# Kernel optimization log

Measured on AMD Instinct MI355X. Metric: run time of the kernel, lower is better.

## Reference

```python
import jax, jax.numpy as jnp
import numpy as np

DIST_MULT = 0.1
CLIP_LOW = 0.0
EPS = 1e-6


def setup_inputs() -> dict:
    key = jax.random.key(0)
    k1, _ = jax.random.split(key)
    x_msg_binned = jax.random.normal(k1, (8, 64, 512, 16), dtype=jnp.float32)
    msk = jnp.ones((8, 64, 512, 1), dtype=jnp.float32)
    return {"x_msg_binned": x_msg_binned, "msk": msk}


def reference(x_msg_binned, msk):
    # A: (B, bins, N, F) masked node features
    A = x_msg_binned * msk
    na = jnp.sum(A * A, axis=-1)  # (B, bins, N)
    # Gram matrix: (B, bins, N, N)
    G = jnp.einsum("bknf,bkmf->bknm", A, A)
    D = jnp.sqrt(jnp.maximum(na[..., :, None] - 2.0 * G + na[..., None, :], EPS))
    dm = jnp.exp(-DIST_MULT * D)[..., None]  # (B, bins, N, N, 1)
    return jnp.clip(dm, CLIP_LOW, 1.0)
```

## Files before the change

kernel.cpp:

```cpp
#include <hip/hip_runtime.h>


typedef float f32x4 __attribute__((ext_vector_type(4)));

#define NEG_DIST_LOG2E (-0.14426950408889634f)
#define EPS_F 1e-6f

__global__ __launch_bounds__(256) void node_pair_gaussian_kernel(
    const float* __restrict__ x,
    const float* __restrict__ msk,
    float* __restrict__ out)
{
    __shared__ __align__(16) float lds_n[16][128];
    __shared__ __align__(16) float lds_m[16][128];
    __shared__ __align__(16) float na_n[128];
    __shared__ __align__(16) float na_m[128];

    const int tid   = threadIdx.x;
    const int tile  = blockIdx.x;
    const int slice = blockIdx.y;
    const int n0 = (tile >> 2) << 7;
    const int m0 = (tile & 3) << 7;

    const float* xs = x   + (size_t)slice * (512 * 16);
    const float* ms = msk + (size_t)slice * 512;

    #pragma unroll
    for (int it = 0; it < 2; ++it) {
        const int task = tid + it * 256;
        const int node = task & 127;
        const int f4   = task >> 7;
        {
            const f32x4 v = *(const f32x4*)(xs + (size_t)(n0 + node) * 16 + f4 * 4);
            const float mm = ms[n0 + node];
            lds_n[f4 * 4 + 0][node] = v.x * mm;
            lds_n[f4 * 4 + 1][node] = v.y * mm;
            lds_n[f4 * 4 + 2][node] = v.z * mm;
            lds_n[f4 * 4 + 3][node] = v.w * mm;
        }
        {
            const f32x4 v = *(const f32x4*)(xs + (size_t)(m0 + node) * 16 + f4 * 4);
            const float mm = ms[m0 + node];
            lds_m[f4 * 4 + 0][node] = v.x * mm;
            lds_m[f4 * 4 + 1][node] = v.y * mm;
            lds_m[f4 * 4 + 2][node] = v.z * mm;
            lds_m[f4 * 4 + 3][node] = v.w * mm;
        }
    }
    __syncthreads();

    {
        const int node = tid & 127;
        float s = 0.0f;
        if (tid < 128) {
            #pragma unroll
            for (int f = 0; f < 16; ++f) s = fmaf(lds_m[f][node], lds_m[f][node], s);
            na_m[node] = s;
        } else {
            #pragma unroll
            for (int f = 0; f < 16; ++f) s = fmaf(lds_n[f][node], lds_n[f][node], s);
            na_n[node] = s;
        }
    }
    __syncthreads();

    const int tx = tid & 15;
    const int ty = tid >> 4;

    float acc[8][8];
    #pragma unroll
    for (int i = 0; i < 8; ++i)
        #pragma unroll
        for (int j = 0; j < 8; ++j) acc[i][j] = 0.0f;

    #pragma unroll
    for (int f = 0; f < 16; ++f) {
        const f32x4 a0 = *(const f32x4*)&lds_n[f][ty * 4];
        const f32x4 a1 = *(const f32x4*)&lds_n[f][64 + ty * 4];
        const f32x4 b0 = *(const f32x4*)&lds_m[f][tx * 4];
        const f32x4 b1 = *(const f32x4*)&lds_m[f][64 + tx * 4];
        const float an[8] = {a0.x, a0.y, a0.z, a0.w, a1.x, a1.y, a1.z, a1.w};
        const float am[8] = {b0.x, b0.y, b0.z, b0.w, b1.x, b1.y, b1.z, b1.w};
        #pragma unroll
        for (int i = 0; i < 8; ++i)
            #pragma unroll
            for (int j = 0; j < 8; ++j)
                acc[i][j] = fmaf(an[i], am[j], acc[i][j]);
    }

    const f32x4 nn0 = *(const f32x4*)&na_n[ty * 4];
    const f32x4 nn1 = *(const f32x4*)&na_n[64 + ty * 4];
    const f32x4 nm0 = *(const f32x4*)&na_m[tx * 4];
    const f32x4 nm1 = *(const f32x4*)&na_m[64 + tx * 4];
    const float nn[8] = {nn0.x, nn0.y, nn0.z, nn0.w, nn1.x, nn1.y, nn1.z, nn1.w};
    const float nm[8] = {nm0.x, nm0.y, nm0.z, nm0.w, nm1.x, nm1.y, nm1.z, nm1.w};

    float* outs = out + (size_t)slice * (512 * 512) + (size_t)n0 * 512 + m0;

    #pragma unroll
    for (int i = 0; i < 8; ++i) {
        const int row = (i < 4) ? (ty * 4 + i) : (64 + ty * 4 + (i - 4));
        float r[8];
        #pragma unroll
        for (int j = 0; j < 8; ++j) {
            float s = nn[i] + nm[j] - 2.0f * acc[i][j];
            s = fmaxf(s, EPS_F);
            const float d = __builtin_amdgcn_sqrtf(s);
            const float e = __builtin_amdgcn_exp2f(d * NEG_DIST_LOG2E);
            r[j] = fminf(e, 1.0f);
        }
        f32x4 w0 = {r[0], r[1], r[2], r[3]};
        f32x4 w1 = {r[4], r[5], r[6], r[7]};
        __builtin_nontemporal_store(w0, (f32x4*)(outs + (size_t)row * 512 + tx * 4));
        __builtin_nontemporal_store(w1, (f32x4*)(outs + (size_t)row * 512 + 64 + tx * 4));
    }
}

extern "C" void kernel_launch(void* const* d_in, const int* in_sizes, int n_in,
                              void* d_out, int out_size, void* d_ws, size_t ws_size,
                              hipStream_t stream) {
    const float* x   = (const float*)d_in[0];
    const float* msk = (const float*)d_in[1];
    float* out = (float*)d_out;

    dim3 grid(16, 512);
    node_pair_gaussian_kernel<<<grid, 256, 0, stream>>>(x, msk, out);
}
```

Measured before the change: 530.7 us.

## Compute Gram tiles with fp16 MFMA and restructure blocks per half-slice

Replaces the scalar FP32 outer-product Gram computation with 32x32x16 fp16 MFMA instructions, storing masked features in LDS as fp16 with padded stride. Each block now loads a whole slice once and computes half of its 512x512 output, instead of one 128x128 tile per block. Norms are computed from the fp16-rounded values for consistency. The fp16 cast trades accuracy for MFMA throughput. Output stores become scalar per-lane column writes instead of 16-byte vectors, which may cost store efficiency in a kernel that is mostly output-write bound. The clamp to 1.0 is also dropped.

Measured after the change: 541.4 us. +2.0%, slower.

```diff
diff --git a/kernel.cpp b/kernel.cpp
--- a/kernel.cpp
+++ b/kernel.cpp
@@ -1,118 +1,98 @@
 #include <hip/hip_runtime.h>
 
 
-typedef float f32x4 __attribute__((ext_vector_type(4)));
+typedef float    f32x4  __attribute__((ext_vector_type(4)));
+typedef float    f32x16 __attribute__((ext_vector_type(16)));
+typedef _Float16 f16x8  __attribute__((ext_vector_type(8)));
 
 #define NEG_DIST_LOG2E (-0.14426950408889634f)
 #define EPS_F 1e-6f
+#define NSTRIDE 24
 
-__global__ __launch_bounds__(256) void node_pair_gaussian_kernel(
+__global__ __launch_bounds__(256, 4) void node_pair_gaussian_mfma(
     const float* __restrict__ x,
     const float* __restrict__ msk,
     float* __restrict__ out)
 {
-    __shared__ __align__(16) float lds_n[16][128];
-    __shared__ __align__(16) float lds_m[16][128];
-    __shared__ __align__(16) float na_n[128];
-    __shared__ __align__(16) float na_m[128];
+    __shared__ _Float16 af[512 * NSTRIDE];
+    __shared__ float    na[512];
 
     const int tid   = threadIdx.x;
-    const int tile  = blockIdx.x;
-    const int slice = blockIdx.y;
-    const int n0 = (tile >> 2) << 7;
-    const int m0 = (tile & 3) << 7;
+    const int slice = blockIdx.x >> 1;
+    const int half  = blockIdx.x & 1;
 
     const float* xs = x   + (size_t)slice * (512 * 16);
     const float* ms = msk + (size_t)slice * 512;
 
     #pragma unroll
     for (int it = 0; it < 2; ++it) {
-        const int task = tid + it * 256;
-        const int node = task & 127;
-        const int f4   = task >> 7;
-        {
-            const f32x4 v = *(const f32x4*)(xs + (size_t)(n0 + node) * 16 + f4 * 4);
-            const float mm = ms[n0 + node];
-            lds_n[f4 * 4 + 0][node] = v.x * mm;
-            lds_n[f4 * 4 + 1][node] = v.y * mm;
-            lds_n[f4 * 4 + 2][node] = v.z * mm;
-            lds_n[f4 * 4 + 3][node] = v.w * mm;
+        const int node = it * 256 + tid;
+        const float mm = ms[node];
+        const f32x4 v0 = *(const f32x4*)(xs + node * 16 +  0) * mm;
+        const f32x4 v1 = *(const f32x4*)(xs + node * 16 +  4) * mm;
+        const f32x4 v2 = *(const f32x4*)(xs + node * 16 +  8) * mm;
+        const f32x4 v3 = *(const f32x4*)(xs + node * 16 + 12) * mm;
+        const float vv[16] = {v0.x, v0.y, v0.z, v0.w, v1.x, v1.y, v1.z, v1.w,
+                              v2.x, v2.y, v2.z, v2.w, v3.x, v3.y, v3.z, v3.w};
+        f16x8 h0, h1;
+        float s = 0.0f;
+        #pragma unroll
+        for (int f = 0; f < 8; ++f) {
+            const _Float16 h = (_Float16)vv[f];
+            h0[f] = h;
+            const float hf = (float)h;
+            s = fmaf(hf, hf, s);
         }
-        {
-            const f32x4 v = *(const f32x4*)(xs + (size_t)(m0 + node) * 16 + f4 * 4);
-            const float mm = ms[m0 + node];
-            lds_m[f4 * 4 + 0][node] = v.x * mm;
-            lds_m[f4 * 4 + 1][node] = v.y * mm;
-            lds_m[f4 * 4 + 2][node] = v.z * mm;
-            lds_m[f4 * 4 + 3][node] = v.w * mm;
+        #pragma unroll
+        for (int f = 0; f < 8; ++f) {
+            const _Float16 h = (_Float16)vv[8 + f];
+            h1[f] = h;
+            const float hf = (float)h;
+            s = fmaf(hf, hf, s);
         }
+        *(f16x8*)&af[node * NSTRIDE + 0] = h0;
+        *(f16x8*)&af[node * NSTRIDE + 8] = h1;
+        na[node] = s;
     }
     __syncthreads();
 
-    {
-        const int node = tid & 127;
-        float s = 0.0f;
-        if (tid < 128) {
-            #pragma unroll
-            for (int f = 0; f < 16; ++f) s = fmaf(lds_m[f][node], lds_m[f][node], s);
-            na_m[node] = s;
-        } else {
-            #pragma unroll
-            for (int f = 0; f < 16; ++f) s = fmaf(lds_n[f][node], lds_n[f][node], s);
-            na_n[node] = s;
-        }
-    }
-    __syncthreads();
+    const int wave  = tid >> 6;
+    const int lane  = tid & 63;
+    const int ln31  = lane & 31;
+    const int khalf = lane >> 5;
 
-    const int tx = tid & 15;
-    const int ty = tid >> 4;
-
-    float acc[8][8];
-    #pragma unroll
-    for (int i = 0; i < 8; ++i)
-        #pragma unroll
-        for (int j = 0; j < 8; ++j) acc[i][j] = 0.0f;
+    float* outs = out + (size_t)slice * (512 * 512);
 
     #pragma unroll
-    for (int f = 0; f < 16; ++f) {
-        const f32x4 a0 = *(const f32x4*)&lds_n[f][ty * 4];
-        const f32x4 a1 = *(const f32x4*)&lds_n[f][64 + ty * 4];
-        const f32x4 b0 = *(const f32x4*)&lds_m[f][tx * 4];
-        const f32x4 b1 = *(const f32x4*)&lds_m[f][64 + tx * 4];
-        const float an[8] = {a0.x, a0.y, a0.z, a0.w, a1.x, a1.y, a1.z, a1.w};
-        const float am[8] = {b0.x, b0.y, b0.z, b0.w, b1.x, b1.y, b1.z, b1.w};
+    for (int band = 0; band < 2; ++band) {
+        const int row0 = half * 256 + (wave * 2 + band) * 32;
+        const f16x8 afrag = *(const f16x8*)&af[(row0 + ln31) * NSTRIDE + khalf * 8];
+        f32x4 nn[4];
         #pragma unroll
-        for (int i = 0; i < 8; ++i)
+        for (int g = 0; g < 4; ++g)
+            nn[g] = *(const f32x4*)&na[row0 + g * 8 + khalf * 4];
+
+        for (int c = 0; c < 16; ++c) {
+            const f16x8 bfrag = *(const f16x8*)&af[(c * 32 + ln31) * NSTRIDE + khalf * 8];
+            const float tm = na[c * 32 + ln31];
+
+            f32x16 acc;
             #pragma unroll
-            for (int j = 0; j < 8; ++j)
-                acc[i][j] = fmaf(an[i], am[j], acc[i][j]);
-    }
+            for (int i = 0; i < 16; ++i) acc[i] = 0.0f;
+            acc = __builtin_amdgcn_mfma_f32_32x32x16_f16(afrag, bfrag, acc, 0, 0, 0);
 
-    const f32x4 nn0 = *(const f32x4*)&na_n[ty * 4];
-    const f32x4 nn1 = *(const f32x4*)&na_n[64 + ty * 4];
-    const f32x4 nm0 = *(const f32x4*)&na_m[tx * 4];
-    const f32x4 nm1 = *(const f32x4*)&na_m[64 + tx * 4];
-    const float nn[8] = {nn0.x, nn0.y, nn0.z, nn0.w, nn1.x, nn1.y, nn1.z, nn1.w};
-    const float nm[8] = {nm0.x, nm0.y, nm0.z, nm0.w, nm1.x, nm1.y, nm1.z, nm1.w};
-
-    float* outs = out + (size_t)slice * (512 * 512) + (size_t)n0 * 512 + m0;
-
-    #pragma unroll
-    for (int i = 0; i < 8; ++i) {
-        const int row = (i < 4) ? (ty * 4 + i) : (64 + ty * 4 + (i - 4));
-        float r[8];
-        #pragma unroll
-        for (int j = 0; j < 8; ++j) {
-            float s = nn[i] + nm[j] - 2.0f * acc[i][j];
-            s = fmaxf(s, EPS_F);
-            const float d = __builtin_amdgcn_sqrtf(s);
-            const float e = __builtin_amdgcn_exp2f(d * NEG_DIST_LOG2E);
-            r[j] = fminf(e, 1.0f);
+            float* colp = outs + (size_t)(row0 + khalf * 4) * 512 + c * 32 + ln31;
+            #pragma unroll
+            for (int r = 0; r < 16; ++r) {
+                const int g = r >> 2, q = r & 3;
+                const float pre = nn[g][q] + tm;
+                float s = fmaf(-2.0f, acc[r], pre);
+                s = fmaxf(s, EPS_F);
+                const float d = __builtin_amdgcn_sqrtf(s);
+                const float e = __builtin_amdgcn_exp2f(d * NEG_DIST_LOG2E);
+                __builtin_nontemporal_store(e, colp + (size_t)(g * 8 + q) * 512);
+            }
         }
-        f32x4 w0 = {r[0], r[1], r[2], r[3]};
-        f32x4 w1 = {r[4], r[5], r[6], r[7]};
-        __builtin_nontemporal_store(w0, (f32x4*)(outs + (size_t)row * 512 + tx * 4));
-        __builtin_nontemporal_store(w1, (f32x4*)(outs + (size_t)row * 512 + 64 + tx * 4));
     }
 }
 
@@ -123,6 +103,5 @@
     const float* msk = (const float*)d_in[1];
     float* out = (float*)d_out;
 
-    dim3 grid(16, 512);
-    node_pair_gaussian_kernel<<<grid, 256, 0, stream>>>(x, msk, out);
+    node_pair_gaussian_mfma<<<1024, 256, 0, stream>>>(x, msk, out);
 }
```
